# Optimization experiments

Measured on AMD Instinct MI355X. Metric: run time of the kernel, lower is better.

Reference implementation:

```python
import jax, jax.numpy as jnp
import numpy as np


def setup_inputs() -> dict:
    key = jax.random.key(0)
    ks = jax.random.split(key, 4)
    B, H, W, C = 4, 64, 64, 256
    Ck = C // 8
    x = jax.random.normal(ks[0], (B, H, W, C), dtype=jnp.float32)
    Wf = jax.random.normal(ks[1], (C, Ck), dtype=jnp.float32) * (1.0 / np.sqrt(C))
    Wg = jax.random.normal(ks[2], (C, Ck), dtype=jnp.float32) * (1.0 / np.sqrt(C))
    Wh = jax.random.normal(ks[3], (C, C), dtype=jnp.float32) * (1.0 / np.sqrt(C))
    bf = jnp.zeros((Ck,), jnp.float32)
    bg = jnp.zeros((Ck,), jnp.float32)
    bh = jnp.zeros((C,), jnp.float32)
    gamma = jnp.ones((1,), jnp.float32)
    return {"x": x, "Wf": Wf, "bf": bf, "Wg": Wg, "bg": bg, "Wh": Wh, "bh": bh, "gamma": gamma}


def reference(x, Wf, bf, Wg, bg, Wh, bh, gamma):
    B, H, W, C = x.shape
    N = H * W
    xf = x.reshape(B, N, C)  # hw_flatten; 1x1 conv == per-pixel matmul
    f = xf @ Wf + bf          # [B, N, C//8] (keys)
    g = xf @ Wg + bg          # [B, N, C//8] (queries)
    h = xf @ Wh + bh          # [B, N, C]    (values)
    s = jnp.einsum('bnk,bmk->bnm', g, f)   # [B, N, N], no scaling (as in source)
    b = jax.nn.softmax(s, axis=-1)
    o = jnp.einsum('bnm,bmc->bnc', b, h)   # [B, N, C]
    y = gamma * o.reshape(B, H, W, C) + x
    return y
```

## Files before the change

### kernel.cpp

```cpp
#include <hip/hip_runtime.h>
#include <stdint.h>

typedef short short8 __attribute__((ext_vector_type(8)));
typedef short short4_t __attribute__((ext_vector_type(4)));
typedef float f32x4 __attribute__((ext_vector_type(4)));

__device__ __forceinline__ float bf2f(unsigned short u) {
    union { unsigned int i; float f; } v; v.i = ((unsigned int)u) << 16; return v.f;
}
__device__ __forceinline__ unsigned short f2bf(float f) {
    union { float f; unsigned int i; } v; v.f = f;
    return (unsigned short)((v.i + 0x8000u) >> 16);
}

__global__ void k_wtrans(const float* __restrict__ Wf,
                         const float* __restrict__ Wg,
                         const float* __restrict__ Wh,
                         unsigned short* __restrict__ wTh,
                         unsigned short* __restrict__ wTl) {
    int col = blockIdx.x;
    int k = threadIdx.x;
    float v;
    if (col < 32) v = Wf[k * 32 + col];
    else if (col < 64) v = Wg[k * 32 + (col - 32)];
    else v = Wh[k * 256 + (col - 64)];
    unsigned short h = f2bf(v);
    wTh[col * 256 + k] = h;
    if (col < 64) wTl[col * 256 + k] = f2bf(v - bf2f(h));
}

__global__ __launch_bounds__(256) void k_proj(
    const float* __restrict__ x,
    const unsigned short* __restrict__ wTh,
    const unsigned short* __restrict__ wTl,
    const float* __restrict__ bfb,
    const float* __restrict__ bgb,
    const float* __restrict__ bhb,
    unsigned short* __restrict__ fKh,
    unsigned short* __restrict__ fKl,
    unsigned short* __restrict__ gQh,
    unsigned short* __restrict__ gQl,
    unsigned short* __restrict__ hT) {
    __shared__ short sm[4 * 64 * 136];
    const int XH = 0, XL = 64 * 136, WH = 2 * 64 * 136, WL = 3 * 64 * 136;
    int tid = threadIdx.x;
    int wave = tid >> 6, lane = tid & 63, lq = lane & 15, quad = lane >> 4;
    int rt = blockIdx.x;
    const float* xbase = x + (size_t)rt * 64 * 256;

    f32x4 zero4 = {0.f, 0.f, 0.f, 0.f};
    f32x4 acc[5][4];
#pragma unroll
    for (int cb = 0; cb < 5; ++cb)
#pragma unroll
        for (int ct = 0; ct < 4; ++ct) acc[cb][ct] = zero4;

    for (int ph = 0; ph < 2; ++ph) {
        int k0 = ph * 128;
        __syncthreads();
#pragma unroll
        for (int u = 0; u < 4; ++u) {
            int q = u * 256 + tid;
            int row = q >> 4, kc = q & 15;
            const float* src = &xbase[row * 256 + k0 + kc * 8];
            f32x4 a0 = *(const f32x4*)src;
            f32x4 a1 = *(const f32x4*)(src + 4);
            short8 sh, sl;
#pragma unroll
            for (int j = 0; j < 4; ++j) {
                unsigned short h0 = f2bf(a0[j]);
                sh[j] = (short)h0; sl[j] = (short)f2bf(a0[j] - bf2f(h0));
                unsigned short h1 = f2bf(a1[j]);
                sh[4 + j] = (short)h1; sl[4 + j] = (short)f2bf(a1[j] - bf2f(h1));
            }
            *(short8*)&sm[XH + row * 136 + kc * 8] = sh;
            *(short8*)&sm[XL + row * 136 + kc * 8] = sl;
        }
        for (int cb = 0; cb < 5; ++cb) {
            __syncthreads();
            int cstart = (cb < 4) ? (64 + cb * 64) : 0;
#pragma unroll
            for (int u = 0; u < 4; ++u) {
                int q = u * 256 + tid;
                int row = q >> 4, kc = q & 15;
                *(short8*)&sm[WH + row * 136 + kc * 8] =
                    *(const short8*)&wTh[(cstart + row) * 256 + k0 + kc * 8];
            }
            if (cb == 4) {
#pragma unroll
                for (int u = 0; u < 4; ++u) {
                    int q = u * 256 + tid;
                    int row = q >> 4, kc = q & 15;
                    *(short8*)&sm[WL + row * 136 + kc * 8] =
                        *(const short8*)&wTl[row * 256 + k0 + kc * 8];
                }
            }
            __syncthreads();
#pragma unroll
            for (int ks = 0; ks < 4; ++ks) {
                short8 ah = *(const short8*)&sm[XH + (wave * 16 + lq) * 136 + ks * 32 + quad * 8];
                short8 al = *(const short8*)&sm[XL + (wave * 16 + lq) * 136 + ks * 32 + quad * 8];
#pragma unroll
                for (int ct = 0; ct < 4; ++ct) {
                    short8 bh = *(const short8*)&sm[WH + (lq + 16 * ct) * 136 + ks * 32 + quad * 8];
                    acc[cb][ct] = __builtin_amdgcn_mfma_f32_16x16x32_bf16(ah, bh, acc[cb][ct], 0, 0, 0);
                    if (cb == 4) {
                        short8 bl = *(const short8*)&sm[WL + (lq + 16 * ct) * 136 + ks * 32 + quad * 8];
                        acc[cb][ct] = __builtin_amdgcn_mfma_f32_16x16x32_bf16(al, bh, acc[cb][ct], 0, 0, 0);
                        acc[cb][ct] = __builtin_amdgcn_mfma_f32_16x16x32_bf16(ah, bl, acc[cb][ct], 0, 0, 0);
                    }
                }
            }
        }
    }

    int rowl = wave * 16 + quad * 4;
    int grow0 = rt * 64;
    int bidx = grow0 >> 12;

#pragma unroll
    for (int cb = 0; cb < 4; ++cb) {
        int n0 = (grow0 & 4095) + rowl;
#pragma unroll
        for (int ct = 0; ct < 4; ++ct) {
            int c = cb * 64 + lq + 16 * ct;
            float bias = bhb[c];
            short4_t pk;
#pragma unroll
            for (int r = 0; r < 4; ++r) pk[r] = (short)f2bf(acc[cb][ct][r] + bias);
            size_t a8 = (((size_t)(bidx * 16 + (c >> 4)) * 128 + (n0 >> 5)) * 64 +
                         ((n0 & 31) >> 3) * 16 + (c & 15)) * 8 + (n0 & 7);
            *(short4_t*)&hT[a8] = pk;
        }
    }

#pragma unroll
    for (int ct = 0; ct < 4; ++ct) {
        int coll = lq + 16 * ct;
#pragma unroll
        for (int r = 0; r < 4; ++r) {
            int grow = grow0 + rowl + r;
            int n = grow & 4095;
            float v = acc[4][ct][r];
            if (coll < 32) {
                size_t o = (size_t)(bidx * 256 + (n >> 4)) * 512 +
                           ((coll >> 3) * 16 + (n & 15)) * 8 + (coll & 7);
                v += bfb[coll];
                unsigned short h = f2bf(v);
                fKh[o] = h;
                fKl[o] = f2bf(v - bf2f(h));
            } else {
                int cg = coll - 32;
                size_t og = (size_t)(bidx * 256 + (n >> 4)) * 512 +
                            ((cg >> 3) * 16 + (n & 15)) * 8 + (cg & 7);
                v += bgb[cg];
                unsigned short h = f2bf(v);
                gQh[og] = h;
                gQl[og] = f2bf(v - bf2f(h));
            }
        }
    }
}

#define PSTR 72
__global__ __launch_bounds__(512, 2) void k_attn(
    const unsigned short* __restrict__ fKh,
    const unsigned short* __restrict__ fKl,
    const unsigned short* __restrict__ gQh,
    const unsigned short* __restrict__ gQl,
    const unsigned short* __restrict__ hT,
    const float* __restrict__ x,
    const float* __restrict__ gam_p,
    float* __restrict__ out) {
    __shared__ short Ps[2][2][64 * PSTR];
    __shared__ float lsum[8][64];
    int tid = threadIdx.x;
    int wave = tid >> 6, lane = tid & 63, lq = lane & 15, quad = lane >> 4;
    int grp = wave >> 2, w = wave & 3;
    int b = blockIdx.x & 3, qt = blockIdx.x >> 2;
    int lchunk = quad * 16 + lq;

    const unsigned short* fhB = fKh + (size_t)b * 131072;
    const unsigned short* flB = fKl + (size_t)b * 131072;
    const unsigned short* hB  = hT + (size_t)b * 1048576;

    f32x4 zero4 = {0.f, 0.f, 0.f, 0.f};
    f32x4 acc[16];
#pragma unroll
    for (int i = 0; i < 16; ++i) acc[i] = zero4;
    float l_part[16];
#pragma unroll
    for (int i = 0; i < 16; ++i) l_part[i] = 0.f;

    short8 gh[4], gl[4];
#pragma unroll
    for (int rb = 0; rb < 4; ++rb) {
        size_t gt = (size_t)(b * 256 + qt * 4 + rb) * 512 + lchunk * 8;
        gh[rb] = *(const short8*)&gQh[gt];
        gl[rb] = *(const short8*)&gQl[gt];
    }

    int ftbase = grp * 128;
    int hkbase = grp * 64;

    for (int kt = 0; kt < 32; ++kt) {
        int p = kt & 1;
        int ftile = ftbase + kt * 4 + w;
        short8 fh = *(const short8*)&fhB[(size_t)ftile * 512 + lchunk * 8];
        short8 fl = *(const short8*)&flB[(size_t)ftile * 512 + lchunk * 8];
        short8 hb[4][2];
#pragma unroll
        for (int ct = 0; ct < 4; ++ct) {
            int ctile = w * 4 + ct;
#pragma unroll
            for (int kk = 0; kk < 2; ++kk) {
                int k32 = hkbase + kt * 2 + kk;
                hb[ct][kk] = *(const short8*)
                    &hB[((size_t)(ctile * 128 + k32) * 64 + lchunk) * 8];
            }
        }

        f32x4 S[4];
#pragma unroll
        for (int rb = 0; rb < 4; ++rb) {
            S[rb] = __builtin_amdgcn_mfma_f32_16x16x32_bf16(gh[rb], fh, zero4, 0, 0, 0);
            S[rb] = __builtin_amdgcn_mfma_f32_16x16x32_bf16(gl[rb], fh, S[rb], 0, 0, 0);
            S[rb] = __builtin_amdgcn_mfma_f32_16x16x32_bf16(gh[rb], fl, S[rb], 0, 0, 0);
        }

#pragma unroll
        for (int rb = 0; rb < 4; ++rb)
#pragma unroll
            for (int r = 0; r < 4; ++r) {
                float e = __expf(S[rb][r]);
                S[rb][r] = e;
                l_part[rb * 4 + r] += e;
            }
#pragma unroll
        for (int rb = 0; rb < 4; ++rb)
#pragma unroll
            for (int r = 0; r < 4; ++r)
                Ps[p][grp][(rb * 16 + quad * 4 + r) * PSTR + w * 16 + lq] =
                    (short)f2bf(S[rb][r]);

        __syncthreads();

#pragma unroll
        for (int rb = 0; rb < 4; ++rb) {
            short8 pa0 = *(const short8*)&Ps[p][grp][(rb * 16 + lq) * PSTR + quad * 8];
            short8 pa1 = *(const short8*)&Ps[p][grp][(rb * 16 + lq) * PSTR + 32 + quad * 8];
#pragma unroll
            for (int ct = 0; ct < 4; ++ct) {
                acc[rb * 4 + ct] = __builtin_amdgcn_mfma_f32_16x16x32_bf16(pa0, hb[ct][0], acc[rb * 4 + ct], 0, 0, 0);
                acc[rb * 4 + ct] = __builtin_amdgcn_mfma_f32_16x16x32_bf16(pa1, hb[ct][1], acc[rb * 4 + ct], 0, 0, 0);
            }
        }
    }

#pragma unroll
    for (int i = 0; i < 16; ++i) {
        float s = l_part[i];
        s += __shfl_xor(s, 1);
        s += __shfl_xor(s, 2);
        s += __shfl_xor(s, 4);
        s += __shfl_xor(s, 8);
        l_part[i] = s;
    }
    if (lq == 0) {
#pragma unroll
        for (int rb = 0; rb < 4; ++rb)
#pragma unroll
            for (int r = 0; r < 4; ++r)
                lsum[wave][rb * 16 + quad * 4 + r] = l_part[rb * 4 + r];
    }
    __syncthreads();

    float* xb = (float*)&Ps[0][0][0];
    for (int rb = 0; rb < 4; ++rb) {
        if (grp == 1) {
#pragma unroll
            for (int ct = 0; ct < 4; ++ct)
#pragma unroll
                for (int r = 0; r < 4; ++r)
                    xb[(quad * 4 + r) * 256 + w * 64 + ct * 16 + lq] = acc[rb * 4 + ct][r];
        }
        __syncthreads();
        if (grp == 0) {
#pragma unroll
            for (int ct = 0; ct < 4; ++ct)
#pragma unroll
                for (int r = 0; r < 4; ++r)
                    acc[rb * 4 + ct][r] += xb[(quad * 4 + r) * 256 + w * 64 + ct * 16 + lq];
        }
        __syncthreads();
    }

    if (grp == 0) {
        float gam = gam_p[0];
#pragma unroll
        for (int rb = 0; rb < 4; ++rb) {
            float linv[4];
#pragma unroll
            for (int r = 0; r < 4; ++r) {
                int row = rb * 16 + quad * 4 + r;
                float lt = 0.f;
#pragma unroll
                for (int wv = 0; wv < 8; ++wv) lt += lsum[wv][row];
                linv[r] = 1.0f / lt;
            }
#pragma unroll
            for (int ct = 0; ct < 4; ++ct) {
                int c = w * 64 + ct * 16 + lq;
#pragma unroll
                for (int r = 0; r < 4; ++r) {
                    int n = qt * 64 + rb * 16 + quad * 4 + r;
                    size_t idx = ((size_t)(b * 4096 + n)) * 256 + c;
                    out[idx] = gam * (acc[rb * 4 + ct][r] * linv[r]) + x[idx];
                }
            }
        }
    }
}

extern "C" void kernel_launch(void* const* d_in, const int* in_sizes, int n_in,
                              void* d_out, int out_size, void* d_ws, size_t ws_size,
                              hipStream_t stream) {
    const float* x   = (const float*)d_in[0];
    const float* Wf  = (const float*)d_in[1];
    const float* bfb = (const float*)d_in[2];
    const float* Wg  = (const float*)d_in[3];
    const float* bgb = (const float*)d_in[4];
    const float* Wh  = (const float*)d_in[5];
    const float* bhb = (const float*)d_in[6];
    const float* gam = (const float*)d_in[7];
    float* out = (float*)d_out;

    char* ws = (char*)d_ws;
    const size_t MI = 1u << 20;
    unsigned short* fKh = (unsigned short*)(ws);
    unsigned short* fKl = (unsigned short*)(ws + 1 * MI);
    unsigned short* gQh = (unsigned short*)(ws + 2 * MI);
    unsigned short* gQl = (unsigned short*)(ws + 3 * MI);
    unsigned short* hT  = (unsigned short*)(ws + 4 * MI);
    unsigned short* wTh = (unsigned short*)(ws + 12 * MI);
    unsigned short* wTl = (unsigned short*)(ws + 12 * MI + 160 * 1024);

    k_wtrans<<<dim3(320), dim3(256), 0, stream>>>(Wf, Wg, Wh, wTh, wTl);
    k_proj<<<dim3(256), dim3(256), 0, stream>>>(x, wTh, wTl, bfb, bgb, bhb,
                                                fKh, fKl, gQh, gQl, hT);
    k_attn<<<dim3(256), dim3(512), 0, stream>>>(fKh, fKl, gQh, gQl, hT,
                                                x, gam, out);
}
```

Measured before the change: 157.0 us.

## Split attention over key halves and projection over column blocks for more parallelism

The projection kernel now launches a 2D grid, with each block handling one 64-column output slice. Only the f/g slice keeps the split-bf16 hi/lo compensation, and the smaller LDS tile allows more blocks per CU. The attention kernel splits the key dimension into two halves across 512 blocks and writes unnormalized partial accumulators and row sums to memory. A new combine kernel then sums the two halves, normalizes, applies gamma and adds the residual. This fills more CUs with work, at the cost of extra global traffic for the fp32 partials and an extra kernel launch.

```diff
diff --git a/kernel.cpp b/kernel.cpp
--- a/kernel.cpp
+++ b/kernel.cpp
@@ -29,7 +29,7 @@
     if (col < 64) wTl[col * 256 + k] = f2bf(v - bf2f(h));
 }
 
-__global__ __launch_bounds__(256) void k_proj(
+__global__ __launch_bounds__(256, 4) void k_proj(
     const float* __restrict__ x,
     const unsigned short* __restrict__ wTh,
     const unsigned short* __restrict__ wTl,
@@ -41,122 +41,130 @@
     unsigned short* __restrict__ gQh,
     unsigned short* __restrict__ gQl,
     unsigned short* __restrict__ hT) {
-    __shared__ short sm[4 * 64 * 136];
-    const int XH = 0, XL = 64 * 136, WH = 2 * 64 * 136, WL = 3 * 64 * 136;
+    __shared__ short sm[4 * 64 * 72];
+    const int XH = 0, XL = 64 * 72, WH = 2 * 64 * 72, WL = 3 * 64 * 72;
     int tid = threadIdx.x;
     int wave = tid >> 6, lane = tid & 63, lq = lane & 15, quad = lane >> 4;
     int rt = blockIdx.x;
     const float* xbase = x + (size_t)rt * 64 * 256;
-
     f32x4 zero4 = {0.f, 0.f, 0.f, 0.f};
-    f32x4 acc[5][4];
-#pragma unroll
-    for (int cb = 0; cb < 5; ++cb)
-#pragma unroll
-        for (int ct = 0; ct < 4; ++ct) acc[cb][ct] = zero4;
-
-    for (int ph = 0; ph < 2; ++ph) {
-        int k0 = ph * 128;
-        __syncthreads();
-#pragma unroll
-        for (int u = 0; u < 4; ++u) {
-            int q = u * 256 + tid;
-            int row = q >> 4, kc = q & 15;
-            const float* src = &xbase[row * 256 + k0 + kc * 8];
-            f32x4 a0 = *(const f32x4*)src;
-            f32x4 a1 = *(const f32x4*)(src + 4);
-            short8 sh, sl;
-#pragma unroll
-            for (int j = 0; j < 4; ++j) {
-                unsigned short h0 = f2bf(a0[j]);
-                sh[j] = (short)h0; sl[j] = (short)f2bf(a0[j] - bf2f(h0));
-                unsigned short h1 = f2bf(a1[j]);
-                sh[4 + j] = (short)h1; sl[4 + j] = (short)f2bf(a1[j] - bf2f(h1));
-            }
-            *(short8*)&sm[XH + row * 136 + kc * 8] = sh;
-            *(short8*)&sm[XL + row * 136 + kc * 8] = sl;
-        }
-        for (int cb = 0; cb < 5; ++cb) {
+    f32x4 acc[4] = {zero4, zero4, zero4, zero4};
+
+    if (blockIdx.y < 4) {
+        int cstart = 64 + blockIdx.y * 64;
+        for (int ph = 0; ph < 4; ++ph) {
+            int k0 = ph * 64;
             __syncthreads();
-            int cstart = (cb < 4) ? (64 + cb * 64) : 0;
-#pragma unroll
-            for (int u = 0; u < 4; ++u) {
+#pragma unroll
+            for (int u = 0; u < 2; ++u) {
                 int q = u * 256 + tid;
-                int row = q >> 4, kc = q & 15;
-                *(short8*)&sm[WH + row * 136 + kc * 8] =
+                int row = q >> 3, kc = q & 7;
+                const float* src = &xbase[row * 256 + k0 + kc * 8];
+                f32x4 a0 = *(const f32x4*)src;
+                f32x4 a1 = *(const f32x4*)(src + 4);
+                short8 s;
+#pragma unroll
+                for (int j = 0; j < 4; ++j) {
+                    s[j] = (short)f2bf(a0[j]);
+                    s[4 + j] = (short)f2bf(a1[j]);
+                }
+                *(short8*)&sm[XH + row * 72 + kc * 8] = s;
+                *(short8*)&sm[WH + row * 72 + kc * 8] =
                     *(const short8*)&wTh[(cstart + row) * 256 + k0 + kc * 8];
             }
-            if (cb == 4) {
-#pragma unroll
-                for (int u = 0; u < 4; ++u) {
-                    int q = u * 256 + tid;
-                    int row = q >> 4, kc = q & 15;
-                    *(short8*)&sm[WL + row * 136 + kc * 8] =
-                        *(const short8*)&wTl[row * 256 + k0 + kc * 8];
-                }
-            }
             __syncthreads();
 #pragma unroll
-            for (int ks = 0; ks < 4; ++ks) {
-                short8 ah = *(const short8*)&sm[XH + (wave * 16 + lq) * 136 + ks * 32 + quad * 8];
-                short8 al = *(const short8*)&sm[XL + (wave * 16 + lq) * 136 + ks * 32 + quad * 8];
+            for (int ks = 0; ks < 2; ++ks) {
+                short8 a = *(const short8*)&sm[XH + (wave * 16 + lq) * 72 + ks * 32 + quad * 8];
 #pragma unroll
                 for (int ct = 0; ct < 4; ++ct) {
-                    short8 bh = *(const short8*)&sm[WH + (lq + 16 * ct) * 136 + ks * 32 + quad * 8];
-                    acc[cb][ct] = __builtin_amdgcn_mfma_f32_16x16x32_bf16(ah, bh, acc[cb][ct], 0, 0, 0);
-                    if (cb == 4) {
-                        short8 bl = *(const short8*)&sm[WL + (lq + 16 * ct) * 136 + ks * 32 + quad * 8];
-                        acc[cb][ct] = __builtin_amdgcn_mfma_f32_16x16x32_bf16(al, bh, acc[cb][ct], 0, 0, 0);
-                        acc[cb][ct] = __builtin_amdgcn_mfma_f32_16x16x32_bf16(ah, bl, acc[cb][ct], 0, 0, 0);
-                    }
-                }
-            }
-        }
-    }
-
-    int rowl = wave * 16 + quad * 4;
-    int grow0 = rt * 64;
-    int bidx = grow0 >> 12;
-
-#pragma unroll
-    for (int cb = 0; cb < 4; ++cb) {
+                    short8 bfr = *(const short8*)&sm[WH + (lq + 16 * ct) * 72 + ks * 32 + quad * 8];
+                    acc[ct] = __builtin_amdgcn_mfma_f32_16x16x32_bf16(a, bfr, acc[ct], 0, 0, 0);
+                }
+            }
+        }
+        int rowl = wave * 16 + quad * 4;
+        int grow0 = rt * 64;
+        int bidx = grow0 >> 12;
         int n0 = (grow0 & 4095) + rowl;
 #pragma unroll
         for (int ct = 0; ct < 4; ++ct) {
-            int c = cb * 64 + lq + 16 * ct;
+            int c = blockIdx.y * 64 + lq + 16 * ct;
             float bias = bhb[c];
             short4_t pk;
 #pragma unroll
-            for (int r = 0; r < 4; ++r) pk[r] = (short)f2bf(acc[cb][ct][r] + bias);
+            for (int r = 0; r < 4; ++r) pk[r] = (short)f2bf(acc[ct][r] + bias);
             size_t a8 = (((size_t)(bidx * 16 + (c >> 4)) * 128 + (n0 >> 5)) * 64 +
                          ((n0 & 31) >> 3) * 16 + (c & 15)) * 8 + (n0 & 7);
             *(short4_t*)&hT[a8] = pk;
         }
-    }
-
-#pragma unroll
-    for (int ct = 0; ct < 4; ++ct) {
-        int coll = lq + 16 * ct;
-#pragma unroll
-        for (int r = 0; r < 4; ++r) {
-            int grow = grow0 + rowl + r;
-            int n = grow & 4095;
-            float v = acc[4][ct][r];
-            if (coll < 32) {
-                size_t o = (size_t)(bidx * 256 + (n >> 4)) * 512 +
-                           ((coll >> 3) * 16 + (n & 15)) * 8 + (coll & 7);
-                v += bfb[coll];
-                unsigned short h = f2bf(v);
-                fKh[o] = h;
-                fKl[o] = f2bf(v - bf2f(h));
-            } else {
-                int cg = coll - 32;
-                size_t og = (size_t)(bidx * 256 + (n >> 4)) * 512 +
-                            ((cg >> 3) * 16 + (n & 15)) * 8 + (cg & 7);
-                v += bgb[cg];
-                unsigned short h = f2bf(v);
-                gQh[og] = h;
-                gQl[og] = f2bf(v - bf2f(h));
+    } else {
+        for (int ph = 0; ph < 4; ++ph) {
+            int k0 = ph * 64;
+            __syncthreads();
+#pragma unroll
+            for (int u = 0; u < 2; ++u) {
+                int q = u * 256 + tid;
+                int row = q >> 3, kc = q & 7;
+                const float* src = &xbase[row * 256 + k0 + kc * 8];
+                f32x4 a0 = *(const f32x4*)src;
+                f32x4 a1 = *(const f32x4*)(src + 4);
+                short8 sh, sl;
+#pragma unroll
+                for (int j = 0; j < 4; ++j) {
+                    unsigned short h0 = f2bf(a0[j]);
+                    sh[j] = (short)h0; sl[j] = (short)f2bf(a0[j] - bf2f(h0));
+                    unsigned short h1 = f2bf(a1[j]);
+                    sh[4 + j] = (short)h1; sl[4 + j] = (short)f2bf(a1[j] - bf2f(h1));
+                }
+                *(short8*)&sm[XH + row * 72 + kc * 8] = sh;
+                *(short8*)&sm[XL + row * 72 + kc * 8] = sl;
+                *(short8*)&sm[WH + row * 72 + kc * 8] =
+                    *(const short8*)&wTh[row * 256 + k0 + kc * 8];
+                *(short8*)&sm[WL + row * 72 + kc * 8] =
+                    *(const short8*)&wTl[row * 256 + k0 + kc * 8];
+            }
+            __syncthreads();
+#pragma unroll
+            for (int ks = 0; ks < 2; ++ks) {
+                short8 ah = *(const short8*)&sm[XH + (wave * 16 + lq) * 72 + ks * 32 + quad * 8];
+                short8 al = *(const short8*)&sm[XL + (wave * 16 + lq) * 72 + ks * 32 + quad * 8];
+#pragma unroll
+                for (int ct = 0; ct < 4; ++ct) {
+                    short8 bh = *(const short8*)&sm[WH + (lq + 16 * ct) * 72 + ks * 32 + quad * 8];
+                    short8 bl = *(const short8*)&sm[WL + (lq + 16 * ct) * 72 + ks * 32 + quad * 8];
+                    acc[ct] = __builtin_amdgcn_mfma_f32_16x16x32_bf16(ah, bh, acc[ct], 0, 0, 0);
+                    acc[ct] = __builtin_amdgcn_mfma_f32_16x16x32_bf16(al, bh, acc[ct], 0, 0, 0);
+                    acc[ct] = __builtin_amdgcn_mfma_f32_16x16x32_bf16(ah, bl, acc[ct], 0, 0, 0);
+                }
+            }
+        }
+        int rowl = wave * 16 + quad * 4;
+        int grow0 = rt * 64;
+        int bidx = grow0 >> 12;
+#pragma unroll
+        for (int ct = 0; ct < 4; ++ct) {
+            int coll = lq + 16 * ct;
+#pragma unroll
+            for (int r = 0; r < 4; ++r) {
+                int n = (grow0 & 4095) + rowl + r;
+                float v = acc[ct][r];
+                if (coll < 32) {
+                    size_t o = (size_t)(bidx * 256 + (n >> 4)) * 512 +
+                               ((coll >> 3) * 16 + (n & 15)) * 8 + (coll & 7);
+                    v += bfb[coll];
+                    unsigned short h = f2bf(v);
+                    fKh[o] = h;
+                    fKl[o] = f2bf(v - bf2f(h));
+                } else {
+                    int cg = coll - 32;
+                    size_t og = (size_t)(bidx * 256 + (n >> 4)) * 512 +
+                                ((cg >> 3) * 16 + (n & 15)) * 8 + (cg & 7);
+                    v += bgb[cg];
+                    unsigned short h = f2bf(v);
+                    gQh[og] = h;
+                    gQl[og] = f2bf(v - bf2f(h));
+                }
             }
         }
     }
@@ -169,20 +177,23 @@
     const unsigned short* __restrict__ gQh,
     const unsigned short* __restrict__ gQl,
     const unsigned short* __restrict__ hT,
-    const float* __restrict__ x,
-    const float* __restrict__ gam_p,
-    float* __restrict__ out) {
+    float* __restrict__ pacc0,
+    float* __restrict__ pacc1,
+    float* __restrict__ pl0,
+    float* __restrict__ pl1) {
     __shared__ short Ps[2][2][64 * PSTR];
     __shared__ float lsum[8][64];
     int tid = threadIdx.x;
     int wave = tid >> 6, lane = tid & 63, lq = lane & 15, quad = lane >> 4;
     int grp = wave >> 2, w = wave & 3;
-    int b = blockIdx.x & 3, qt = blockIdx.x >> 2;
+    int b = blockIdx.x & 3, qt = (blockIdx.x >> 2) & 63, ks = blockIdx.x >> 8;
     int lchunk = quad * 16 + lq;
 
     const unsigned short* fhB = fKh + (size_t)b * 131072;
     const unsigned short* flB = fKl + (size_t)b * 131072;
     const unsigned short* hB  = hT + (size_t)b * 1048576;
+    float* pacc = ks ? pacc1 : pacc0;
+    float* pl   = ks ? pl1 : pl0;
 
     f32x4 zero4 = {0.f, 0.f, 0.f, 0.f};
     f32x4 acc[16];
@@ -200,10 +211,10 @@
         gl[rb] = *(const short8*)&gQl[gt];
     }
 
-    int ftbase = grp * 128;
-    int hkbase = grp * 64;
-
-    for (int kt = 0; kt < 32; ++kt) {
+    int ftbase = ks * 128 + grp * 64;
+    int hkbase = ks * 64 + grp * 32;
+
+    for (int kt = 0; kt < 16; ++kt) {
         int p = kt & 1;
         int ftile = ftbase + kt * 4 + w;
         short8 fh = *(const short8*)&fhB[(size_t)ftile * 512 + lchunk * 8];
@@ -275,6 +286,13 @@
     }
     __syncthreads();
 
+    if (tid < 64) {
+        float lt = 0.f;
+#pragma unroll
+        for (int wv = 0; wv < 8; ++wv) lt += lsum[wv][tid];
+        pl[b * 4096 + qt * 64 + tid] = lt;
+    }
+
     float* xb = (float*)&Ps[0][0][0];
     for (int rb = 0; rb < 4; ++rb) {
         if (grp == 1) {
@@ -296,30 +314,38 @@
     }
 
     if (grp == 0) {
-        float gam = gam_p[0];
-#pragma unroll
-        for (int rb = 0; rb < 4; ++rb) {
-            float linv[4];
-#pragma unroll
-            for (int r = 0; r < 4; ++r) {
-                int row = rb * 16 + quad * 4 + r;
-                float lt = 0.f;
-#pragma unroll
-                for (int wv = 0; wv < 8; ++wv) lt += lsum[wv][row];
-                linv[r] = 1.0f / lt;
-            }
+#pragma unroll
+        for (int rb = 0; rb < 4; ++rb)
 #pragma unroll
             for (int ct = 0; ct < 4; ++ct) {
                 int c = w * 64 + ct * 16 + lq;
 #pragma unroll
                 for (int r = 0; r < 4; ++r) {
                     int n = qt * 64 + rb * 16 + quad * 4 + r;
-                    size_t idx = ((size_t)(b * 4096 + n)) * 256 + c;
-                    out[idx] = gam * (acc[rb * 4 + ct][r] * linv[r]) + x[idx];
-                }
-            }
-        }
-    }
+                    pacc[((size_t)(b * 4096 + n)) * 256 + c] = acc[rb * 4 + ct][r];
+                }
+            }
+    }
+}
+
+__global__ __launch_bounds__(256) void k_combine(
+    const float* __restrict__ x,
+    const float* __restrict__ gam_p,
+    const float* __restrict__ pacc1,
+    const float* __restrict__ pl0,
+    const float* __restrict__ pl1,
+    float* __restrict__ out) {
+    int gid = blockIdx.x * 256 + threadIdx.x;
+    int row = gid >> 6;
+    f32x4 a0 = *(const f32x4*)&out[(size_t)gid * 4];
+    f32x4 a1 = *(const f32x4*)&pacc1[(size_t)gid * 4];
+    f32x4 xv = *(const f32x4*)&x[(size_t)gid * 4];
+    float linv = 1.0f / (pl0[row] + pl1[row]);
+    float gam = gam_p[0];
+    f32x4 o;
+#pragma unroll
+    for (int j = 0; j < 4; ++j) o[j] = gam * ((a0[j] + a1[j]) * linv) + xv[j];
+    *(f32x4*)&out[(size_t)gid * 4] = o;
 }
 
 extern "C" void kernel_launch(void* const* d_in, const int* in_sizes, int n_in,
@@ -344,10 +370,14 @@
     unsigned short* hT  = (unsigned short*)(ws + 4 * MI);
     unsigned short* wTh = (unsigned short*)(ws + 12 * MI);
     unsigned short* wTl = (unsigned short*)(ws + 12 * MI + 160 * 1024);
+    float* pacc1 = (float*)(ws + 13 * MI);
+    float* pl0   = (float*)(ws + 29 * MI);
+    float* pl1   = (float*)(ws + 29 * MI + 64 * 1024);
 
     k_wtrans<<<dim3(320), dim3(256), 0, stream>>>(Wf, Wg, Wh, wTh, wTl);
-    k_proj<<<dim3(256), dim3(256), 0, stream>>>(x, wTh, wTl, bfb, bgb, bhb,
-                                                fKh, fKl, gQh, gQl, hT);
-    k_attn<<<dim3(256), dim3(512), 0, stream>>>(fKh, fKl, gQh, gQl, hT,
-                                                x, gam, out);
-}
+    k_proj<<<dim3(256, 5), dim3(256), 0, stream>>>(x, wTh, wTl, bfb, bgb, bhb,
+                                                   fKh, fKl, gQh, gQl, hT);
+    k_attn<<<dim3(512), dim3(512), 0, stream>>>(fKh, fKl, gQh, gQl, hT,
+                                                out, pacc1, pl0, pl1);
+    k_combine<<<dim3(4096), dim3(256), 0, stream>>>(x, gam, pacc1, pl0, pl1, out);
+}
```

After: 159.8 us. Within noise of the previous version (+1.8%).
